# Kernel tuning notes

Hardware: AMD Instinct MI355X
Metric: run time of the kernel (lower is better)

The kernel has to match this reference:

```python
import jax, jax.numpy as jnp
import numpy as np

N_NODES = 50000
N_EDGES = 1600000
N_FEAT = 128
EMB = 128
N_CLASSES = 10
N_GRAPHS = 512


def setup_inputs() -> dict:
    key = jax.random.key(0)
    ks = jax.random.split(key, 12)
    x = jax.random.normal(ks[0], (N_NODES, N_FEAT), dtype=jnp.float32)
    edge_index = jax.random.randint(ks[1], (2, N_EDGES), 0, N_NODES, dtype=jnp.int64)
    batch = jnp.sort(jax.random.randint(ks[2], (N_NODES,), 0, N_GRAPHS, dtype=jnp.int64))
    def glorot(k, fan_in, fan_out):
        lim = jnp.sqrt(6.0 / (fan_in + fan_out)).astype(jnp.float32)
        return jax.random.uniform(k, (fan_in, fan_out), jnp.float32, -lim, lim)
    W0 = glorot(ks[3], N_FEAT, EMB); b0 = jnp.zeros((EMB,), jnp.float32)
    W1 = glorot(ks[4], EMB, EMB);    b1 = jnp.zeros((EMB,), jnp.float32)
    W2 = glorot(ks[5], EMB, EMB);    b2 = jnp.zeros((EMB,), jnp.float32)
    Wout = glorot(ks[6], EMB, N_CLASSES)
    bout = jnp.zeros((N_CLASSES,), jnp.float32)
    return {"x": x, "edge_index": edge_index, "batch": batch,
            "W0": W0, "b0": b0, "W1": W1, "b1": b1, "W2": W2, "b2": b2,
            "Wout": Wout, "bout": bout}


def _gcn_conv(x, W, b, src, dst, norm, n_nodes):
    # PyG GCNConv: h = x @ W; aggregate norm * h[src] into dst; add bias.
    h = x @ W                                  # [N, out]
    msg = h[src] * norm[:, None]               # [E+N, out] gather (incl. self-loops)
    out = jax.ops.segment_sum(msg, dst, num_segments=n_nodes)
    return out + b


def reference(x, edge_index, batch, W0, b0, W1, b1, W2, b2, Wout, bout):
    n_nodes = x.shape[0]
    # add self-loops (GCNConv default add_self_loops=True)
    loops = jnp.arange(n_nodes, dtype=edge_index.dtype)
    src = jnp.concatenate([edge_index[0], loops])
    dst = jnp.concatenate([edge_index[1], loops])
    # symmetric normalization D^{-1/2} (A+I) D^{-1/2}
    deg = jax.ops.segment_sum(jnp.ones_like(dst, dtype=x.dtype), dst,
                              num_segments=n_nodes)
    deg_inv_sqrt = jnp.where(deg > 0, jax.lax.rsqrt(jnp.maximum(deg, 1.0)), 0.0)
    norm = deg_inv_sqrt[src] * deg_inv_sqrt[dst]   # [E+N]
    out = jnp.tanh(_gcn_conv(x, W0, b0, src, dst, norm, n_nodes))
    out = jnp.tanh(_gcn_conv(out, W1, b1, src, dst, norm, n_nodes))
    out = _gcn_conv(out, W2, b2, src, dst, norm, n_nodes)
    # global mean pool over per-node graph ids
    sums = jax.ops.segment_sum(out, batch, num_segments=N_GRAPHS)
    counts = jax.ops.segment_sum(jnp.ones((n_nodes,), out.dtype), batch,
                                 num_segments=N_GRAPHS)
    pooled = sums / jnp.maximum(counts, 1.0)[:, None]   # [G, EMB]
    logits = pooled @ Wout + bout                        # [G, C]
    return jax.nn.log_softmax(logits, axis=1)
```

## Files before the change

kernel.cpp:

```cpp
#include <hip/hip_runtime.h>
#include <math.h>


#define BLK_EDGES 4096
#define MAXB 128
#define ECAP 2048
#define WS_STRIDE 136

typedef __attribute__((ext_vector_type(8))) short bf16x8;
typedef __attribute__((ext_vector_type(4))) float f32x4;
typedef __attribute__((ext_vector_type(2))) float f32x2;

static __device__ inline unsigned short f2bf(float f) {
    unsigned u = __float_as_uint(f);
    unsigned r = (u + 0x7FFFu + ((u >> 16) & 1u)) >> 16;
    return (unsigned short)r;
}
static __device__ inline float bf_lo(unsigned u) { return __uint_as_float(u << 16); }
static __device__ inline float bf_hi(unsigned u) { return __uint_as_float(u & 0xFFFF0000u); }
static __device__ inline unsigned char f2fp8(float v) {
    v = fminf(fmaxf(v, -240.f), 240.f);
    int u = __builtin_amdgcn_cvt_pk_fp8_f32(v, v, 0, false);
    return (unsigned char)(u & 0xFF);
}

__global__ __launch_bounds__(256) void blk_hist_prep(const int* __restrict__ dst,
        int* __restrict__ histT, int E, int NBLK, int NB,
        const float* __restrict__ W0, const float* __restrict__ W1,
        const float* __restrict__ W2, unsigned short* __restrict__ wt0,
        unsigned short* __restrict__ wt1, unsigned short* __restrict__ wt2) {
    __shared__ int h[MAXB];
    int blk = blockIdx.x, t = threadIdx.x;
    if (blk >= NBLK) {
        int i = (blk - NBLK) * 256 + t;
        int w = i >> 14, j = i & 16383;
        int k = j >> 7, n2 = j & 127;
        const float* Wp = (w == 0) ? W0 : (w == 1) ? W1 : W2;
        unsigned short* Wt = (w == 0) ? wt0 : (w == 1) ? wt1 : wt2;
        Wt[n2 * 128 + k] = f2bf(Wp[k * 128 + n2]);
        return;
    }
    for (int i = t; i < NB; i += 256) h[i] = 0;
    __syncthreads();
    int lo = blk * BLK_EDGES;
    int hi = min(E, lo + BLK_EDGES);
    for (int i = lo + t; i < hi; i += 256)
        atomicAdd(&h[dst[i] >> 9], 1);
    __syncthreads();
    for (int i = t; i < NB; i += 256) histT[i * NBLK + blk] = h[i];
}

__global__ void scan_block(const int* __restrict__ cnt, int* __restrict__ off,
                           int* __restrict__ bsum, int n) {
    __shared__ int lds[256];
    int t = threadIdx.x;
    int i = blockIdx.x * 256 + t;
    int v = (i < n) ? cnt[i] : 0;
    lds[t] = v;
    __syncthreads();
    for (int d = 1; d < 256; d <<= 1) {
        int add = (t >= d) ? lds[t - d] : 0;
        __syncthreads();
        lds[t] += add;
        __syncthreads();
    }
    if (i < n) off[i] = lds[t] - v;
    if (t == 255) bsum[blockIdx.x] = lds[255];
}

__global__ void scan_top(const int* __restrict__ bsum, int* __restrict__ boff,
                         int nblocks) {
    __shared__ int lds[256];
    int t = threadIdx.x;
    int v = (t < nblocks) ? bsum[t] : 0;
    lds[t] = v;
    __syncthreads();
    for (int d = 1; d < 256; d <<= 1) {
        int add = (t >= d) ? lds[t - d] : 0;
        __syncthreads();
        lds[t] += add;
        __syncthreads();
    }
    if (t < nblocks) boff[t] = lds[t] - v;
}

__global__ __launch_bounds__(256) void scatter_packed(const int* __restrict__ src,
        const int* __restrict__ dst, const int* __restrict__ P,
        const int* __restrict__ boff, unsigned* __restrict__ packed,
        int E, int NBLK, int NB) {
    __shared__ int cur[MAXB];
    int blk = blockIdx.x, t = threadIdx.x;
    for (int i = t; i < NB; i += 256) {
        int idx = i * NBLK + blk;
        cur[i] = P[idx] + boff[idx >> 8];
    }
    __syncthreads();
    int lo = blk * BLK_EDGES;
    int hi = min(E, lo + BLK_EDGES);
    for (int i = lo + t; i < hi; i += 256) {
        int d = dst[i];
        int pos = atomicAdd(&cur[d >> 9], 1);
        packed[pos] = ((unsigned)d << 16) | (unsigned)src[i];
    }
}

__global__ __launch_bounds__(256) void bucket_build(const unsigned* __restrict__ packed,
        const int* __restrict__ P, const int* __restrict__ boff, int* __restrict__ off,
        float* __restrict__ dis, unsigned short* __restrict__ csr16,
        int E, int NBLK, int N, int NB) {
    __shared__ int cnt[512];
    __shared__ int loc[512];
    __shared__ int ps[256];
    int b = blockIdx.x, t = threadIdx.x;
    int i0 = b * NBLK, i1 = (b + 1) * NBLK;
    int start = P[i0] + boff[i0 >> 8];
    int end   = (b == NB - 1) ? E : (P[i1] + boff[i1 >> 8]);
    cnt[t] = 0; cnt[t + 256] = 0;
    __syncthreads();
    for (int i = start + t; i < end; i += 256)
        atomicAdd(&cnt[(packed[i] >> 16) & 511], 1);
    __syncthreads();
    int c0 = cnt[2 * t], c1 = cnt[2 * t + 1];
    ps[t] = c0 + c1;
    __syncthreads();
    for (int d = 1; d < 256; d <<= 1) {
        int add = (t >= d) ? ps[t - d] : 0;
        __syncthreads();
        ps[t] += add;
        __syncthreads();
    }
    int pexcl = ps[t] - (c0 + c1);
    loc[2 * t]     = start + pexcl;
    loc[2 * t + 1] = start + pexcl + c0;
    __syncthreads();
    int node0 = b * 512;
    for (int l = t; l < 512; l += 256) {
        int node = node0 + l;
        if (node < N) {
            off[node] = loc[l];
            dis[node] = rsqrtf((float)cnt[l] + 1.0f);
        }
    }
    if (b == NB - 1 && t == 0) off[N] = E;
    __syncthreads();
    for (int i = start + t; i < end; i += 256) {
        unsigned p = packed[i];
        int l = (p >> 16) & 511;
        int pos = atomicAdd(&loc[l], 1);
        csr16[pos] = (unsigned short)(p & 0xFFFFu);
    }
}

template<int IN_F32>
__global__ __launch_bounds__(128) void gemm_mfma(const void* __restrict__ Av,
        const unsigned short* __restrict__ Wt, const float* __restrict__ dis,
        unsigned char* __restrict__ Hs8, int n) {
    __shared__ unsigned short Ws[128 * WS_STRIDE];
    int t = threadIdx.x;
    for (int i = t; i < 128 * 16; i += 128) {
        int r = i >> 4, j = i & 15;
        uint4 u = ((const uint4*)(Wt + r * 128))[j];
        *(uint4*)&Ws[r * WS_STRIDE + j * 8] = u;
    }
    __syncthreads();

    int wave = t >> 6, lane = t & 63;
    int quad = lane >> 4, l16 = lane & 15;
    int row0 = blockIdx.x * 64 + wave * 32;

    int ra0 = row0 + l16;      if (ra0 >= n) ra0 = n - 1;
    int ra1 = row0 + 16 + l16; if (ra1 >= n) ra1 = n - 1;

    f32x4 acc[2][8];
    const f32x4 z = {0.f, 0.f, 0.f, 0.f};
#pragma unroll
    for (int mi = 0; mi < 2; ++mi)
#pragma unroll
        for (int ni = 0; ni < 8; ++ni) acc[mi][ni] = z;

#pragma unroll
    for (int ks = 0; ks < 4; ++ks) {
        int kof = ks * 32 + quad * 8;
        bf16x8 a0, a1;
        if (IN_F32) {
            const float* A0 = (const float*)Av + (size_t)ra0 * 128 + kof;
            const float* A1 = (const float*)Av + (size_t)ra1 * 128 + kof;
            float4 p0 = ((const float4*)A0)[0], p1 = ((const float4*)A0)[1];
            float4 q0 = ((const float4*)A1)[0], q1 = ((const float4*)A1)[1];
            a0[0] = (short)f2bf(p0.x); a0[1] = (short)f2bf(p0.y);
            a0[2] = (short)f2bf(p0.z); a0[3] = (short)f2bf(p0.w);
            a0[4] = (short)f2bf(p1.x); a0[5] = (short)f2bf(p1.y);
            a0[6] = (short)f2bf(p1.z); a0[7] = (short)f2bf(p1.w);
            a1[0] = (short)f2bf(q0.x); a1[1] = (short)f2bf(q0.y);
            a1[2] = (short)f2bf(q0.z); a1[3] = (short)f2bf(q0.w);
            a1[4] = (short)f2bf(q1.x); a1[5] = (short)f2bf(q1.y);
            a1[6] = (short)f2bf(q1.z); a1[7] = (short)f2bf(q1.w);
        } else {
            a0 = *(const bf16x8*)((const unsigned short*)Av + (size_t)ra0 * 128 + kof);
            a1 = *(const bf16x8*)((const unsigned short*)Av + (size_t)ra1 * 128 + kof);
        }
        bf16x8 b[8];
#pragma unroll
        for (int ni = 0; ni < 8; ++ni)
            b[ni] = *(const bf16x8*)&Ws[(ni * 16 + l16) * WS_STRIDE + kof];
#pragma unroll
        for (int ni = 0; ni < 8; ++ni) {
            acc[0][ni] = __builtin_amdgcn_mfma_f32_16x16x32_bf16(a0, b[ni], acc[0][ni], 0, 0, 0);
            acc[1][ni] = __builtin_amdgcn_mfma_f32_16x16x32_bf16(a1, b[ni], acc[1][ni], 0, 0, 0);
        }
    }
#pragma unroll
    for (int mi = 0; mi < 2; ++mi) {
        int rb = row0 + mi * 16 + quad * 4;
#pragma unroll
        for (int reg = 0; reg < 4; ++reg) {
            int r = rb + reg;
            if (r < n) {
                float dv = dis[r];
#pragma unroll
                for (int ni = 0; ni < 8; ++ni)
                    Hs8[(size_t)r * 128 + ni * 16 + l16] = f2fp8(acc[mi][ni][reg] * dv);
            }
        }
    }
}

template<int DO_TANH>
__global__ __launch_bounds__(256) void aggregate3(const unsigned char* __restrict__ hs,
    const unsigned short* __restrict__ csr, const int* __restrict__ off,
    const float* __restrict__ dis, const float* __restrict__ bias,
    unsigned* __restrict__ outp, int n) {
    __shared__ unsigned short eidx[ECAP];
    int t = threadIdx.x;
    int node0 = blockIdx.x * 4;
    int b0 = off[node0];
    int top = node0 + 4 < n ? node0 + 4 : n;
    int b4 = off[top];
    int mblk = b4 - b0;
    bool staged = (mblk <= ECAP);
    if (staged)
        for (int i = t; i < mblk; i += 256) eidx[i] = csr[b0 + i];
    __syncthreads();

    int node = node0 + (t >> 6);
    if (node >= n) return;
    int lane = t & 63;
    int g = lane >> 4;
    int fq = lane & 15;
    const uint2* H2 = (const uint2*)hs;

    int e0 = off[node];
    int e1 = off[node + 1];
    int le0 = e0 - b0;
    int m = e1 - e0;
    float a0 = 0.f, a1 = 0.f, a2 = 0.f, a3 = 0.f;
    float a4 = 0.f, a5 = 0.f, a6 = 0.f, a7 = 0.f;

    uint2 va[8], vb[8];
    auto cadd = [&](uint2 v) {
        f32x2 p0 = __builtin_amdgcn_cvt_pk_f32_fp8((int)v.x, false);
        f32x2 p1 = __builtin_amdgcn_cvt_pk_f32_fp8((int)v.x, true);
        f32x2 p2 = __builtin_amdgcn_cvt_pk_f32_fp8((int)v.y, false);
        f32x2 p3 = __builtin_amdgcn_cvt_pk_f32_fp8((int)v.y, true);
        a0 += p0.x; a1 += p0.y; a2 += p1.x; a3 += p1.y;
        a4 += p2.x; a5 += p2.y; a6 += p3.x; a7 += p3.y;
    };
    auto sumB = [&](uint2* v) {
#pragma unroll
        for (int j = 0; j < 8; ++j) cadd(v[j]);
    };
    auto loadL = [&](int i, uint2* v) {
#pragma unroll
        for (int j = 0; j < 8; ++j) {
            int e = i + g + 4 * j;
            uint2 val; val.x = 0u; val.y = 0u;
            if (e < m) val = H2[(size_t)eidx[le0 + e] * 16 + fq];
            v[j] = val;
        }
    };
    auto loadG = [&](int i, uint2* v) {
#pragma unroll
        for (int j = 0; j < 8; ++j) {
            int e = i + g + 4 * j;
            uint2 val; val.x = 0u; val.y = 0u;
            if (e < m) val = H2[(size_t)csr[e0 + e] * 16 + fq];
            v[j] = val;
        }
    };

    int B = (m + 31) >> 5;
    if (B) {
        if (staged) {
            loadL(0, va);
            int k = 1;
            for (; k + 1 < B; k += 2) {
                loadL(k << 5, vb);       sumB(va);
                loadL((k + 1) << 5, va); sumB(vb);
            }
            if (k < B) { loadL(k << 5, vb); sumB(va); sumB(vb); }
            else       { sumB(va); }
        } else {
            loadG(0, va);
            int k = 1;
            for (; k + 1 < B; k += 2) {
                loadG(k << 5, vb);       sumB(va);
                loadG((k + 1) << 5, va); sumB(vb);
            }
            if (k < B) { loadG(k << 5, vb); sumB(va); sumB(vb); }
            else       { sumB(va); }
        }
    }

    a0 += __shfl_xor(a0, 32, 64); a0 += __shfl_xor(a0, 16, 64);
    a1 += __shfl_xor(a1, 32, 64); a1 += __shfl_xor(a1, 16, 64);
    a2 += __shfl_xor(a2, 32, 64); a2 += __shfl_xor(a2, 16, 64);
    a3 += __shfl_xor(a3, 32, 64); a3 += __shfl_xor(a3, 16, 64);
    a4 += __shfl_xor(a4, 32, 64); a4 += __shfl_xor(a4, 16, 64);
    a5 += __shfl_xor(a5, 32, 64); a5 += __shfl_xor(a5, 16, 64);
    a6 += __shfl_xor(a6, 32, 64); a6 += __shfl_xor(a6, 16, 64);
    a7 += __shfl_xor(a7, 32, 64); a7 += __shfl_xor(a7, 16, 64);

    if (g == 0) {
        uint2 sv = H2[(size_t)node * 16 + fq];
        cadd(sv);

        float dn = dis[node];
        float4 bv0 = ((const float4*)bias)[2 * fq];
        float4 bv1 = ((const float4*)bias)[2 * fq + 1];
        float o0 = fmaf(dn, a0, bv0.x);
        float o1 = fmaf(dn, a1, bv0.y);
        float o2 = fmaf(dn, a2, bv0.z);
        float o3 = fmaf(dn, a3, bv0.w);
        float o4 = fmaf(dn, a4, bv1.x);
        float o5 = fmaf(dn, a5, bv1.y);
        float o6 = fmaf(dn, a6, bv1.z);
        float o7 = fmaf(dn, a7, bv1.w);
        if (DO_TANH) {
            o0 = tanhf(o0); o1 = tanhf(o1); o2 = tanhf(o2); o3 = tanhf(o3);
            o4 = tanhf(o4); o5 = tanhf(o5); o6 = tanhf(o6); o7 = tanhf(o7);
        }
        uint4 o;
        o.x = (unsigned)f2bf(o0) | ((unsigned)f2bf(o1) << 16);
        o.y = (unsigned)f2bf(o2) | ((unsigned)f2bf(o3) << 16);
        o.z = (unsigned)f2bf(o4) | ((unsigned)f2bf(o5) << 16);
        o.w = (unsigned)f2bf(o6) | ((unsigned)f2bf(o7) << 16);
        *(uint4*)(outp + (size_t)node * 64 + fq * 4) = o;
    }
}

__global__ __launch_bounds__(256) void pool_head(const unsigned* __restrict__ actb,
    const int* __restrict__ batch, const float* __restrict__ Wout,
    const float* __restrict__ bout, float* __restrict__ out, int n, int C) {
    __shared__ float psum[4][128];
    __shared__ float l[16];
    __shared__ float stats[2];
    int g = blockIdx.x;
    int t = threadIdx.x;
    int w = t >> 6;
    int lane = t & 63;
    int lo = 0, hi = n;
    while (lo < hi) { int mid = (lo + hi) >> 1; if (batch[mid] < g) lo = mid + 1; else hi = mid; }
    int lo1 = lo, hi1 = n;
    while (lo1 < hi1) { int mid = (lo1 + hi1) >> 1; if (batch[mid] < g + 1) lo1 = mid + 1; else hi1 = mid; }
    float ax = 0.f, ay = 0.f;
    for (int i = lo + w; i < lo1; i += 4) {
        unsigned v = actb[(size_t)i * 64 + lane];
        ax += bf_lo(v);
        ay += bf_hi(v);
    }
    psum[w][2 * lane]     = ax;
    psum[w][2 * lane + 1] = ay;
    __syncthreads();
    if (w == 0) {
        int cnt = lo1 - lo;
        float inv = 1.0f / (float)(cnt > 0 ? cnt : 1);
        float sx = (psum[0][2 * lane] + psum[1][2 * lane])
                 + (psum[2][2 * lane] + psum[3][2 * lane]);
        float sy = (psum[0][2 * lane + 1] + psum[1][2 * lane + 1])
                 + (psum[2][2 * lane + 1] + psum[3][2 * lane + 1]);
        psum[0][2 * lane]     = sx * inv;
        psum[0][2 * lane + 1] = sy * inv;
    }
    __syncthreads();
    if (t < C) {
        float acc = bout[t];
        for (int f = 0; f < 128; ++f)
            acc = fmaf(psum[0][f], Wout[(size_t)f * C + t], acc);
        l[t] = acc;
    }
    __syncthreads();
    if (t == 0) {
        float m = -1e30f;
        for (int c = 0; c < C; ++c) m = fmaxf(m, l[c]);
        float s = 0.f;
        for (int c = 0; c < C; ++c) s += expf(l[c] - m);
        stats[0] = m;
        stats[1] = logf(s);
    }
    __syncthreads();
    if (t < C) out[(size_t)g * C + t] = l[t] - stats[0] - stats[1];
}

extern "C" void kernel_launch(void* const* d_in, const int* in_sizes, int n_in,
                              void* d_out, int out_size, void* d_ws, size_t ws_size,
                              hipStream_t stream) {
    const float* x     = (const float*)d_in[0];
    const int*   edge  = (const int*)d_in[1];
    const int*   batch = (const int*)d_in[2];
    const float* W0 = (const float*)d_in[3];
    const float* b0 = (const float*)d_in[4];
    const float* W1 = (const float*)d_in[5];
    const float* b1 = (const float*)d_in[6];
    const float* W2 = (const float*)d_in[7];
    const float* b2 = (const float*)d_in[8];
    const float* Wout = (const float*)d_in[9];
    const float* bout = (const float*)d_in[10];
    float* out = (float*)d_out;

    const int N = in_sizes[0] / 128;
    const int E = in_sizes[1] / 2;
    const int C = in_sizes[10];
    const int G = out_size / C;

    const int* src = edge;
    const int* dst = edge + E;

    const int NBLK = (E + BLK_EDGES - 1) / BLK_EDGES;
    const int NB   = (N + 511) / 512;
    const int NBQ  = NB * NBLK;
    const int PREPB = (3 * 16384) / 256;

    char* p = (char*)d_ws;
    auto alloc = [&](size_t bytes) -> void* {
        void* r = (void*)p;
        p += (bytes + 255) & ~(size_t)255;
        return r;
    };
    unsigned char* hs = (unsigned char*)alloc((size_t)N * 128);
    unsigned* actb = (unsigned*)alloc((size_t)N * 128 * 2);
    float* dis    = (float*)alloc((size_t)N * 4);
    int*   off    = (int*)alloc((size_t)(N + 1) * 4);
    int*   P      = (int*)alloc((size_t)(NBQ + 1) * 4);
    int*   bsum   = (int*)alloc(256 * 4);
    int*   boff   = (int*)alloc(256 * 4);
    unsigned* packed = (unsigned*)alloc((size_t)E * 4);
    unsigned short* csr16 = (unsigned short*)alloc((size_t)E * 2);
    unsigned short* wt0 = (unsigned short*)alloc(128 * 128 * 2);
    unsigned short* wt1 = (unsigned short*)alloc(128 * 128 * 2);
    unsigned short* wt2 = (unsigned short*)alloc(128 * 128 * 2);

    const int sb = (NBQ + 255) / 256;

    blk_hist_prep<<<NBLK + PREPB, 256, 0, stream>>>(dst, P, E, NBLK, NB,
                                                    W0, W1, W2, wt0, wt1, wt2);
    scan_block<<<sb, 256, 0, stream>>>(P, P, bsum, NBQ);
    scan_top<<<1, 256, 0, stream>>>(bsum, boff, sb);
    scatter_packed<<<NBLK, 256, 0, stream>>>(src, dst, P, boff, packed, E, NBLK, NB);
    bucket_build<<<NB, 256, 0, stream>>>(packed, P, boff, off, dis, csr16, E, NBLK, N, NB);

    const int gb = (N + 63) / 64;
    const int ab = (N + 3) / 4;

    gemm_mfma<1><<<gb, 128, 0, stream>>>(x,    wt0, dis, hs, N);
    aggregate3<1><<<ab, 256, 0, stream>>>(hs, csr16, off, dis, b0, actb, N);
    gemm_mfma<0><<<gb, 128, 0, stream>>>(actb, wt1, dis, hs, N);
    aggregate3<1><<<ab, 256, 0, stream>>>(hs, csr16, off, dis, b1, actb, N);
    gemm_mfma<0><<<gb, 128, 0, stream>>>(actb, wt2, dis, hs, N);
    aggregate3<0><<<ab, 256, 0, stream>>>(hs, csr16, off, dis, b2, actb, N);

    pool_head<<<G, 256, 0, stream>>>(actb, batch, Wout, bout, out, N, C);
}
```

Measured before the change: 343.1 us.

## Make aggregation persistent: each wave walks a contiguous chunk of nodes

The aggregation kernel previously launched one block per 4 nodes and staged each block's CSR indices in LDS behind a barrier. It now launches a fixed grid of 2048 blocks in which each wave processes a contiguous range of about 6 nodes. The edge-offset reads chain from one node to the next, the bias is loaded once per wave, and the LDS staging and __syncthreads are removed. The load batch per step shrinks from 32 to 16 edges, and launch bounds now request 8 blocks per CU. The aim is lower launch, barrier and per-node setup cost, at the price of less memory-level parallelism per wave and possible imbalance when node degrees vary.

New measurement: 399.2 us. 16.3% more time.

```diff
diff --git a/kernel.cpp b/kernel.cpp
--- a/kernel.cpp
+++ b/kernel.cpp
@@ -4,7 +4,6 @@
 
 #define BLK_EDGES 4096
 #define MAXB 128
-#define ECAP 2048
 #define WS_STRIDE 136
 
 typedef __attribute__((ext_vector_type(8))) short bf16x8;
@@ -226,125 +225,102 @@
 }
 
 template<int DO_TANH>
-__global__ __launch_bounds__(256) void aggregate3(const unsigned char* __restrict__ hs,
+__global__ __launch_bounds__(256, 8) void aggregate3(const unsigned char* __restrict__ hs,
     const unsigned short* __restrict__ csr, const int* __restrict__ off,
     const float* __restrict__ dis, const float* __restrict__ bias,
-    unsigned* __restrict__ outp, int n) {
-    __shared__ unsigned short eidx[ECAP];
+    unsigned* __restrict__ outp, int n, int nwaves) {
     int t = threadIdx.x;
-    int node0 = blockIdx.x * 4;
-    int b0 = off[node0];
-    int top = node0 + 4 < n ? node0 + 4 : n;
-    int b4 = off[top];
-    int mblk = b4 - b0;
-    bool staged = (mblk <= ECAP);
-    if (staged)
-        for (int i = t; i < mblk; i += 256) eidx[i] = csr[b0 + i];
-    __syncthreads();
-
-    int node = node0 + (t >> 6);
-    if (node >= n) return;
+    int wid = blockIdx.x * 4 + (t >> 6);
     int lane = t & 63;
     int g = lane >> 4;
     int fq = lane & 15;
-    const uint2* H2 = (const uint2*)hs;
+    unsigned fob = (unsigned)fq << 3;
+
+    int chunk = (n + nwaves - 1) / nwaves;
+    int node = wid * chunk;
+    int nhi = node + chunk; if (nhi > n) nhi = n;
+    if (node >= nhi) return;
+
+    float4 bv0 = ((const float4*)bias)[2 * fq];
+    float4 bv1 = ((const float4*)bias)[2 * fq + 1];
 
     int e0 = off[node];
-    int e1 = off[node + 1];
-    int le0 = e0 - b0;
-    int m = e1 - e0;
-    float a0 = 0.f, a1 = 0.f, a2 = 0.f, a3 = 0.f;
-    float a4 = 0.f, a5 = 0.f, a6 = 0.f, a7 = 0.f;
-
-    uint2 va[8], vb[8];
-    auto cadd = [&](uint2 v) {
-        f32x2 p0 = __builtin_amdgcn_cvt_pk_f32_fp8((int)v.x, false);
-        f32x2 p1 = __builtin_amdgcn_cvt_pk_f32_fp8((int)v.x, true);
-        f32x2 p2 = __builtin_amdgcn_cvt_pk_f32_fp8((int)v.y, false);
-        f32x2 p3 = __builtin_amdgcn_cvt_pk_f32_fp8((int)v.y, true);
-        a0 += p0.x; a1 += p0.y; a2 += p1.x; a3 += p1.y;
-        a4 += p2.x; a5 += p2.y; a6 += p3.x; a7 += p3.y;
-    };
-    auto sumB = [&](uint2* v) {
-#pragma unroll
-        for (int j = 0; j < 8; ++j) cadd(v[j]);
-    };
-    auto loadL = [&](int i, uint2* v) {
-#pragma unroll
-        for (int j = 0; j < 8; ++j) {
-            int e = i + g + 4 * j;
-            uint2 val; val.x = 0u; val.y = 0u;
-            if (e < m) val = H2[(size_t)eidx[le0 + e] * 16 + fq];
-            v[j] = val;
-        }
-    };
-    auto loadG = [&](int i, uint2* v) {
-#pragma unroll
-        for (int j = 0; j < 8; ++j) {
-            int e = i + g + 4 * j;
-            uint2 val; val.x = 0u; val.y = 0u;
-            if (e < m) val = H2[(size_t)csr[e0 + e] * 16 + fq];
-            v[j] = val;
-        }
-    };
-
-    int B = (m + 31) >> 5;
-    if (B) {
-        if (staged) {
-            loadL(0, va);
+    for (; node < nhi; ++node) {
+        int e1 = off[node + 1];
+        int m = e1 - e0;
+        uint2 sv = *(const uint2*)(hs + (((unsigned)node) << 7) + fob);
+
+        float a0 = 0.f, a1 = 0.f, a2 = 0.f, a3 = 0.f;
+        float a4 = 0.f, a5 = 0.f, a6 = 0.f, a7 = 0.f;
+        auto cadd = [&](uint2 v) {
+            f32x2 p0 = __builtin_amdgcn_cvt_pk_f32_fp8((int)v.x, false);
+            f32x2 p1 = __builtin_amdgcn_cvt_pk_f32_fp8((int)v.x, true);
+            f32x2 p2 = __builtin_amdgcn_cvt_pk_f32_fp8((int)v.y, false);
+            f32x2 p3 = __builtin_amdgcn_cvt_pk_f32_fp8((int)v.y, true);
+            a0 += p0.x; a1 += p0.y; a2 += p1.x; a3 += p1.y;
+            a4 += p2.x; a5 += p2.y; a6 += p3.x; a7 += p3.y;
+        };
+        uint2 va[4], vb[4];
+        auto sumB = [&](uint2* v) {
+#pragma unroll
+            for (int j = 0; j < 4; ++j) cadd(v[j]);
+        };
+        auto loadB = [&](int i, uint2* v) {
+#pragma unroll
+            for (int j = 0; j < 4; ++j) {
+                int e = i + g + 4 * j;
+                uint2 val; val.x = 0u; val.y = 0u;
+                if (e < m)
+                    val = *(const uint2*)(hs +
+                          (((unsigned)csr[e0 + e]) << 7) + fob);
+                v[j] = val;
+            }
+        };
+
+        int B = (m + 15) >> 4;
+        if (B) {
+            loadB(0, va);
             int k = 1;
             for (; k + 1 < B; k += 2) {
-                loadL(k << 5, vb);       sumB(va);
-                loadL((k + 1) << 5, va); sumB(vb);
+                loadB(k << 4, vb);       sumB(va);
+                loadB((k + 1) << 4, va); sumB(vb);
             }
-            if (k < B) { loadL(k << 5, vb); sumB(va); sumB(vb); }
+            if (k < B) { loadB(k << 4, vb); sumB(va); sumB(vb); }
             else       { sumB(va); }
-        } else {
-            loadG(0, va);
-            int k = 1;
-            for (; k + 1 < B; k += 2) {
-                loadG(k << 5, vb);       sumB(va);
-                loadG((k + 1) << 5, va); sumB(vb);
+        }
+
+        a0 += __shfl_xor(a0, 32, 64); a0 += __shfl_xor(a0, 16, 64);
+        a1 += __shfl_xor(a1, 32, 64); a1 += __shfl_xor(a1, 16, 64);
+        a2 += __shfl_xor(a2, 32, 64); a2 += __shfl_xor(a2, 16, 64);
+        a3 += __shfl_xor(a3, 32, 64); a3 += __shfl_xor(a3, 16, 64);
+        a4 += __shfl_xor(a4, 32, 64); a4 += __shfl_xor(a4, 16, 64);
+        a5 += __shfl_xor(a5, 32, 64); a5 += __shfl_xor(a5, 16, 64);
+        a6 += __shfl_xor(a6, 32, 64); a6 += __shfl_xor(a6, 16, 64);
+        a7 += __shfl_xor(a7, 32, 64); a7 += __shfl_xor(a7, 16, 64);
+
+        if (g == 0) {
+            cadd(sv);
+            float dn = dis[node];
+            float o0 = fmaf(dn, a0, bv0.x);
+            float o1 = fmaf(dn, a1, bv0.y);
+            float o2 = fmaf(dn, a2, bv0.z);
+            float o3 = fmaf(dn, a3, bv0.w);
+            float o4 = fmaf(dn, a4, bv1.x);
+            float o5 = fmaf(dn, a5, bv1.y);
+            float o6 = fmaf(dn, a6, bv1.z);
+            float o7 = fmaf(dn, a7, bv1.w);
+            if (DO_TANH) {
+                o0 = tanhf(o0); o1 = tanhf(o1); o2 = tanhf(o2); o3 = tanhf(o3);
+                o4 = tanhf(o4); o5 = tanhf(o5); o6 = tanhf(o6); o7 = tanhf(o7);
             }
-            if (k < B) { loadG(k << 5, vb); sumB(va); sumB(vb); }
-            else       { sumB(va); }
-        }
-    }
-
-    a0 += __shfl_xor(a0, 32, 64); a0 += __shfl_xor(a0, 16, 64);
-    a1 += __shfl_xor(a1, 32, 64); a1 += __shfl_xor(a1, 16, 64);
-    a2 += __shfl_xor(a2, 32, 64); a2 += __shfl_xor(a2, 16, 64);
-    a3 += __shfl_xor(a3, 32, 64); a3 += __shfl_xor(a3, 16, 64);
-    a4 += __shfl_xor(a4, 32, 64); a4 += __shfl_xor(a4, 16, 64);
-    a5 += __shfl_xor(a5, 32, 64); a5 += __shfl_xor(a5, 16, 64);
-    a6 += __shfl_xor(a6, 32, 64); a6 += __shfl_xor(a6, 16, 64);
-    a7 += __shfl_xor(a7, 32, 64); a7 += __shfl_xor(a7, 16, 64);
-
-    if (g == 0) {
-        uint2 sv = H2[(size_t)node * 16 + fq];
-        cadd(sv);
-
-        float dn = dis[node];
-        float4 bv0 = ((const float4*)bias)[2 * fq];
-        float4 bv1 = ((const float4*)bias)[2 * fq + 1];
-        float o0 = fmaf(dn, a0, bv0.x);
-        float o1 = fmaf(dn, a1, bv0.y);
-        float o2 = fmaf(dn, a2, bv0.z);
-        float o3 = fmaf(dn, a3, bv0.w);
-        float o4 = fmaf(dn, a4, bv1.x);
-        float o5 = fmaf(dn, a5, bv1.y);
-        float o6 = fmaf(dn, a6, bv1.z);
-        float o7 = fmaf(dn, a7, bv1.w);
-        if (DO_TANH) {
-            o0 = tanhf(o0); o1 = tanhf(o1); o2 = tanhf(o2); o3 = tanhf(o3);
-            o4 = tanhf(o4); o5 = tanhf(o5); o6 = tanhf(o6); o7 = tanhf(o7);
-        }
-        uint4 o;
-        o.x = (unsigned)f2bf(o0) | ((unsigned)f2bf(o1) << 16);
-        o.y = (unsigned)f2bf(o2) | ((unsigned)f2bf(o3) << 16);
-        o.z = (unsigned)f2bf(o4) | ((unsigned)f2bf(o5) << 16);
-        o.w = (unsigned)f2bf(o6) | ((unsigned)f2bf(o7) << 16);
-        *(uint4*)(outp + (size_t)node * 64 + fq * 4) = o;
+            uint4 o;
+            o.x = (unsigned)f2bf(o0) | ((unsigned)f2bf(o1) << 16);
+            o.y = (unsigned)f2bf(o2) | ((unsigned)f2bf(o3) << 16);
+            o.z = (unsigned)f2bf(o4) | ((unsigned)f2bf(o5) << 16);
+            o.w = (unsigned)f2bf(o6) | ((unsigned)f2bf(o7) << 16);
+            *(uint4*)(outp + (size_t)node * 64 + fq * 4) = o;
+        }
+        e0 = e1;
     }
 }
 
@@ -459,14 +435,16 @@
     bucket_build<<<NB, 256, 0, stream>>>(packed, P, boff, off, dis, csr16, E, NBLK, N, NB);
 
     const int gb = (N + 63) / 64;
-    const int ab = (N + 3) / 4;
+
+    const int AGGB = 2048;
+    const int NWAVES = AGGB * 4;
 
     gemm_mfma<1><<<gb, 128, 0, stream>>>(x,    wt0, dis, hs, N);
-    aggregate3<1><<<ab, 256, 0, stream>>>(hs, csr16, off, dis, b0, actb, N);
+    aggregate3<1><<<AGGB, 256, 0, stream>>>(hs, csr16, off, dis, b0, actb, N, NWAVES);
     gemm_mfma<0><<<gb, 128, 0, stream>>>(actb, wt1, dis, hs, N);
-    aggregate3<1><<<ab, 256, 0, stream>>>(hs, csr16, off, dis, b1, actb, N);
+    aggregate3<1><<<AGGB, 256, 0, stream>>>(hs, csr16, off, dis, b1, actb, N, NWAVES);
     gemm_mfma<0><<<gb, 128, 0, stream>>>(actb, wt2, dis, hs, N);
-    aggregate3<0><<<ab, 256, 0, stream>>>(hs, csr16, off, dis, b2, actb, N);
+    aggregate3<0><<<AGGB, 256, 0, stream>>>(hs, csr16, off, dis, b2, actb, N, NWAVES);
 
     pool_head<<<G, 256, 0, stream>>>(actb, batch, Wout, bout, out, N, C);
 }
```
